# Kernel optimization log

Hardware: AMD Instinct MI355X
Metric: run time of the kernel (lower is better)

The kernel has to match this reference:

```python
import jax, jax.numpy as jnp
import numpy as np

B, D = 16384, 4096
K_SEL = 512  # number of features kept (top-k)


def setup_inputs() -> dict:
    key = jax.random.key(0)
    kx, kk = jax.random.split(key)
    x = jax.random.normal(kx, (B, D), dtype=jnp.float32)
    # kernel initialized ~ RandomUniform(0.999999, 0.9999999); use uniform in that band
    kernel = jax.random.uniform(kk, (D,), dtype=jnp.float32,
                                minval=0.999999, maxval=0.9999999)
    return {"x": x, "kernel": kernel, "k": K_SEL}


def reference(x, kernel, k):
    # selection=True branch: zero out all kernel entries below the k-th largest
    topk_vals, _ = jax.lax.top_k(kernel, k)
    kth_largest = topk_vals[-1]
    kernel_sel = jnp.where(kernel < kth_largest, jnp.zeros_like(kernel), kernel)
    # K.dot(x, tensor_diag(kernel)) == x * kernel (broadcast over batch)
    return x * kernel_sel
```

## Files before the change

### kernel.cpp

```cpp
#include <hip/hip_runtime.h>

typedef float f32x4 __attribute__((ext_vector_type(4)));

__global__ void __launch_bounds__(256)
select_threshold_kernel(const float* __restrict__ kern,
                        const int* __restrict__ kptr,
                        float* __restrict__ sel,
                        int D) {
    const int tid  = threadIdx.x;
    const int lane = tid & 63;
    const int wid  = tid >> 6;

    __shared__ unsigned int s_umin[4], s_umax[4];
    __shared__ int s_cnt[4];

    unsigned int u[16];
    #pragma unroll
    for (int j = 0; j < 16; ++j) {
        int i = tid + j * 256;
        if (i < D) {
            unsigned int b = __float_as_uint(kern[i]);
            u[j] = b ^ (unsigned int)(((int)b >> 31) | (int)0x80000000);
        } else {
            u[j] = 0u;
        }
    }

    unsigned int umin = 0xFFFFFFFFu, umax = 0u;
    #pragma unroll
    for (int j = 0; j < 16; ++j) {
        int i = tid + j * 256;
        if (i < D) { umin = min(umin, u[j]); umax = max(umax, u[j]); }
    }
    #pragma unroll
    for (int off = 32; off; off >>= 1) {
        umin = min(umin, (unsigned int)__shfl_down((int)umin, off, 64));
        umax = max(umax, (unsigned int)__shfl_down((int)umax, off, 64));
    }
    if (lane == 0) { s_umin[wid] = umin; s_umax[wid] = umax; }
    __syncthreads();
    umin = min(min(s_umin[0], s_umin[1]), min(s_umin[2], s_umin[3]));
    umax = max(max(s_umax[0], s_umax[1]), max(s_umax[2], s_umax[3]));

    const int kk = *kptr;
    unsigned int t;
    unsigned int xorv = umin ^ umax;
    if (xorv == 0u) {
        t = umax;
    } else {
        int hb = 31 - __builtin_clz(xorv);
        unsigned int lowmask = (hb == 31) ? 0xFFFFFFFFu : ((1u << (hb + 1)) - 1u);
        t = umax & ~lowmask;
        for (int bit = hb; bit >= 0; --bit) {
            unsigned int cand = t | (1u << bit);
            int c = 0;
            #pragma unroll
            for (int j = 0; j < 16; ++j) c += (u[j] >= cand) ? 1 : 0;
            #pragma unroll
            for (int off = 32; off; off >>= 1) c += __shfl_down(c, off, 64);
            __syncthreads();
            if (lane == 0) s_cnt[wid] = c;
            __syncthreads();
            c = s_cnt[0] + s_cnt[1] + s_cnt[2] + s_cnt[3];
            if (c >= kk) t = cand;
        }
    }

    float thr = __uint_as_float((t & 0x80000000u) ? (t ^ 0x80000000u) : ~t);

    #pragma unroll
    for (int j = 0; j < 16; ++j) {
        int i = tid + j * 256;
        if (i < D) {
            float v = kern[i];
            sel[i] = (v < thr) ? 0.0f : v;
        }
    }
}

__global__ void __launch_bounds__(256)
bcast_mul_kernel(const f32x4* __restrict__ x,
                 const f32x4* __restrict__ sel,
                 f32x4* __restrict__ out,
                 int n4, int d4mask) {
    int idx = blockIdx.x * blockDim.x + threadIdx.x;
    int stride = gridDim.x * blockDim.x;
    for (int i = idx; i < n4; i += stride) {
        f32x4 xv = __builtin_nontemporal_load(&x[i]);
        f32x4 sv = sel[i & d4mask];
        f32x4 o = xv * sv;
        __builtin_nontemporal_store(o, &out[i]);
    }
}

extern "C" void kernel_launch(void* const* d_in, const int* in_sizes, int n_in,
                              void* d_out, int out_size, void* d_ws, size_t ws_size,
                              hipStream_t stream) {
    const float* x    = (const float*)d_in[0];
    const float* kern = (const float*)d_in[1];
    const int*   kptr = (const int*)d_in[2];
    float* out = (float*)d_out;
    float* sel = (float*)d_ws;

    const int D = in_sizes[1];

    select_threshold_kernel<<<1, 256, 0, stream>>>(kern, kptr, sel, D);

    const int n4 = out_size / 4;
    const int d4mask = (D / 4) - 1;
    const int blocks = 2048;
    bcast_mul_kernel<<<blocks, 256, 0, stream>>>(
        (const f32x4*)x, (const f32x4*)sel, (f32x4*)out, n4, d4mask);
}
```

Before: 104.9 us.

## Fuse top-k threshold selection into broadcast multiply kernel

Every block of the multiply kernel now recomputes the top-k threshold redundantly via the radix bit search, removing the single-block select kernel, its launch and the serial dependency before the multiply. When the grid stride is a multiple of D/4, each thread builds its selected kernel vector once and keeps it in registers, and the streaming loop is unrolled by four. In exchange every one of the 2048 blocks repeats the 4096-element load and a roughly 30-iteration count loop with block barriers, which adds latency before streaming starts.

```diff
diff --git a/kernel.cpp b/kernel.cpp
--- a/kernel.cpp
+++ b/kernel.cpp
@@ -3,10 +3,12 @@
 typedef float f32x4 __attribute__((ext_vector_type(4)));
 
 __global__ void __launch_bounds__(256)
-select_threshold_kernel(const float* __restrict__ kern,
-                        const int* __restrict__ kptr,
-                        float* __restrict__ sel,
-                        int D) {
+fused_select_mul(const f32x4* __restrict__ x,
+                 const float* __restrict__ kern,
+                 const int* __restrict__ kptr,
+                 f32x4* __restrict__ out,
+                 int D, int n4)
+{
     const int tid  = threadIdx.x;
     const int lane = tid & 63;
     const int wid  = tid >> 6;
@@ -65,31 +67,47 @@
             if (c >= kk) t = cand;
         }
     }
+    const float thr = __uint_as_float((t & 0x80000000u) ? (t ^ 0x80000000u) : ~t);
 
-    float thr = __uint_as_float((t & 0x80000000u) ? (t ^ 0x80000000u) : ~t);
+    const int gid    = blockIdx.x * 256 + tid;
+    const int stride = gridDim.x * 256;
+    const int d4mask = (D >> 2) - 1;
+    const f32x4* kern4 = (const f32x4*)kern;
 
-    #pragma unroll
-    for (int j = 0; j < 16; ++j) {
-        int i = tid + j * 256;
-        if (i < D) {
-            float v = kern[i];
-            sel[i] = (v < thr) ? 0.0f : v;
+    if ((stride & d4mask) == 0) {
+        f32x4 kv = kern4[gid & d4mask];
+        f32x4 sv;
+        sv.x = (kv.x < thr) ? 0.0f : kv.x;
+        sv.y = (kv.y < thr) ? 0.0f : kv.y;
+        sv.z = (kv.z < thr) ? 0.0f : kv.z;
+        sv.w = (kv.w < thr) ? 0.0f : kv.w;
+
+        int i = gid;
+        for (; i + 3 * stride < n4; i += 4 * stride) {
+            f32x4 a0 = __builtin_nontemporal_load(&x[i]);
+            f32x4 a1 = __builtin_nontemporal_load(&x[i + stride]);
+            f32x4 a2 = __builtin_nontemporal_load(&x[i + 2 * stride]);
+            f32x4 a3 = __builtin_nontemporal_load(&x[i + 3 * stride]);
+            __builtin_nontemporal_store(a0 * sv, &out[i]);
+            __builtin_nontemporal_store(a1 * sv, &out[i + stride]);
+            __builtin_nontemporal_store(a2 * sv, &out[i + 2 * stride]);
+            __builtin_nontemporal_store(a3 * sv, &out[i + 3 * stride]);
         }
-    }
-}
-
-__global__ void __launch_bounds__(256)
-bcast_mul_kernel(const f32x4* __restrict__ x,
-                 const f32x4* __restrict__ sel,
-                 f32x4* __restrict__ out,
-                 int n4, int d4mask) {
-    int idx = blockIdx.x * blockDim.x + threadIdx.x;
-    int stride = gridDim.x * blockDim.x;
-    for (int i = idx; i < n4; i += stride) {
-        f32x4 xv = __builtin_nontemporal_load(&x[i]);
-        f32x4 sv = sel[i & d4mask];
-        f32x4 o = xv * sv;
-        __builtin_nontemporal_store(o, &out[i]);
+        for (; i < n4; i += stride) {
+            f32x4 a = __builtin_nontemporal_load(&x[i]);
+            __builtin_nontemporal_store(a * sv, &out[i]);
+        }
+    } else {
+        for (int i = gid; i < n4; i += stride) {
+            f32x4 kv = kern4[i & d4mask];
+            f32x4 sv;
+            sv.x = (kv.x < thr) ? 0.0f : kv.x;
+            sv.y = (kv.y < thr) ? 0.0f : kv.y;
+            sv.z = (kv.z < thr) ? 0.0f : kv.z;
+            sv.w = (kv.w < thr) ? 0.0f : kv.w;
+            f32x4 a = __builtin_nontemporal_load(&x[i]);
+            __builtin_nontemporal_store(a * sv, &out[i]);
+        }
     }
 }
 
@@ -100,15 +118,11 @@
     const float* kern = (const float*)d_in[1];
     const int*   kptr = (const int*)d_in[2];
     float* out = (float*)d_out;
-    float* sel = (float*)d_ws;
 
-    const int D = in_sizes[1];
+    const int D  = in_sizes[1];
+    const int n4 = out_size / 4;
 
-    select_threshold_kernel<<<1, 256, 0, stream>>>(kern, kptr, sel, D);
-
-    const int n4 = out_size / 4;
-    const int d4mask = (D / 4) - 1;
     const int blocks = 2048;
-    bcast_mul_kernel<<<blocks, 256, 0, stream>>>(
-        (const f32x4*)x, (const f32x4*)sel, (f32x4*)out, n4, d4mask);
+    fused_select_mul<<<blocks, 256, 0, stream>>>(
+        (const f32x4*)x, kern, kptr, (f32x4*)out, D, n4);
 }
```

Result: slower. 126.2 us (+20.3%).
